# Optimization experiments

Hardware: AMD Instinct MI355X
Metric: run time of the kernel (lower is better)

## Reference

```python
import jax, jax.numpy as jnp
import numpy as np

NUM_HEADS = 16
WINDOW = 64


def setup_inputs() -> dict:
    key = jax.random.key(0)
    ks = jax.random.split(key, 6)
    b, l, d = 2, 2048, 1024
    s = 1.0 / np.sqrt(d)
    return {
        "x": jax.random.normal(ks[0], (b, l, d), dtype=jnp.float32),
        "Wq": jax.random.normal(ks[1], (d, d), dtype=jnp.float32) * s,
        "Wk": jax.random.normal(ks[2], (d, d), dtype=jnp.float32) * s,
        "Wv": jax.random.normal(ks[3], (d, d), dtype=jnp.float32) * s,
        "Wo": jax.random.normal(ks[4], (d, d), dtype=jnp.float32) * s,
        "bo": jax.random.normal(ks[5], (d,), dtype=jnp.float32) * 0.01,
    }


def reference(x, Wq, Wk, Wv, Wo, bo):
    b, l, d = x.shape
    h, w = NUM_HEADS, WINDOW
    dh = d // h
    p = w // 2
    # Projections. Padding is zeros and proj_k/proj_v have no bias, so
    # padding-then-projecting equals projecting-then-zero-padding.
    q = (x @ Wq.T).reshape(b, l, h, dh)                     # (b,l,h,dh)
    xp = jnp.pad(x, ((0, 0), (p, p), (0, 0)))               # (b,l+2p,d)
    k = (xp @ Wk.T).reshape(b, l + 2 * p, h, dh)
    v = (xp @ Wv.T).reshape(b, l + 2 * p, h, dh)
    # Sliding windows: query i attends to padded positions i .. i+w-1
    win_idx = jnp.arange(l)[:, None] + jnp.arange(w)[None, :]  # (l,w)
    kw = k[:, win_idx]                                       # (b,l,w,h,dh)
    vw = v[:, win_idx]                                       # (b,l,w,h,dh)
    scale = 1.0 / np.float32(np.sqrt(dh))
    scores = jnp.einsum('blhd,blwhd->blhw', q, kw) * scale   # (b,l,h,w)
    attn = jax.nn.softmax(scores, axis=-1)
    out = jnp.einsum('blhw,blwhd->blhd', attn, vw).reshape(b, l, d)
    return out @ Wo.T + bo
```

## Files before the change

### kernel.cpp

```cpp
#include <hip/hip_runtime.h>
#include <hip/hip_bf16.h>
#include <cstdint>

typedef __bf16 bf16;
typedef __bf16 bf16x4 __attribute__((ext_vector_type(4)));
typedef __bf16 bf16x8 __attribute__((ext_vector_type(8)));
typedef float floatx4 __attribute__((ext_vector_type(4)));

typedef __attribute__((address_space(1))) void as1_void;
typedef __attribute__((address_space(3))) void as3_void;

__device__ __forceinline__ void gld16(const void* g, void* l) {
#if __has_builtin(__builtin_amdgcn_global_load_lds)
  __builtin_amdgcn_global_load_lds((as1_void*)(uintptr_t)g, (as3_void*)l, 16, 0, 0);
#else
  *(uint4*)l = *(const uint4*)g;
#endif
}

__global__ __launch_bounds__(256) void convert_kernel(
    const float* __restrict__ x, const float* __restrict__ wq,
    const float* __restrict__ wk, const float* __restrict__ wv,
    const float* __restrict__ wo, bf16* __restrict__ xbf,
    bf16* __restrict__ wqkv, bf16* __restrict__ wob) {
  int i = blockIdx.x * 256 + threadIdx.x;
  const float* src;
  bf16* dst;
  int off;
  if (i < 1048576) {
    src = x; dst = xbf; off = i;
  } else if (i < 1310720) {
    src = wq; dst = wqkv; off = i - 1048576;
  } else if (i < 1572864) {
    src = wk; dst = wqkv + 1048576; off = i - 1310720;
  } else if (i < 1835008) {
    src = wv; dst = wqkv + 2097152; off = i - 1572864;
  } else {
    src = wo; dst = wob; off = i - 1835008;
  }
  float4 v = ((const float4*)src)[off];
  bf16x4 o;
  o[0] = (bf16)v.x; o[1] = (bf16)v.y; o[2] = (bf16)v.z; o[3] = (bf16)v.w;
  ((bf16x4*)dst)[off] = o;
}

template <int MODE, int BN>
__global__ __launch_bounds__(256) void gemm_nt(const bf16* __restrict__ A,
                                               const bf16* __restrict__ Bm,
                                               bf16* __restrict__ Cb,
                                               float* __restrict__ Cf,
                                               const float* __restrict__ bias,
                                               int M, int N, int K) {
  constexpr int WN = BN / 2;
  constexpr int NI = WN / 16;
  __shared__ __attribute__((aligned(16))) bf16 As[128 * 32];
  __shared__ __attribute__((aligned(16))) bf16 Bs[BN * 32];
  const int tid = threadIdx.x;
  const int lane = tid & 63;
  const int wave = tid >> 6;
  const int quad = lane >> 4;
  const int n0 = lane & 15;
  const int wm = wave >> 1;
  const int wn = wave & 1;
  const int nwg = gridDim.x * gridDim.y;
  const int nid = blockIdx.y * gridDim.x + blockIdx.x;
  int sid = nid;
  if ((nwg & 7) == 0) sid = (nid & 7) * (nwg >> 3) + (nid >> 3);
  const int bN = sid % gridDim.x, bM = sid / gridDim.x;
  const bf16* Ab = A + (size_t)bM * 128 * K;
  const bf16* Bb = Bm + (size_t)bN * BN * K;
  const int c0 = tid, c1 = tid + 256;
  floatx4 acc[4][NI] = {};
  for (int k0 = 0; k0 < K; k0 += 32) {
    gld16(Ab + (size_t)(c0 >> 2) * K + k0 + (c0 & 3) * 8, &As[c0 * 8]);
    gld16(Ab + (size_t)(c1 >> 2) * K + k0 + (c1 & 3) * 8, &As[c1 * 8]);
#pragma unroll
    for (int cc = 0; cc < BN * 4; cc += 256) {
      const int c = cc + tid;
      gld16(Bb + (size_t)(c >> 2) * K + k0 + (c & 3) * 8, &Bs[c * 8]);
    }
    __syncthreads();
    bf16x8 af[4], bfr[NI];
#pragma unroll
    for (int mi = 0; mi < 4; ++mi)
      af[mi] = *(const bf16x8*)&As[(wm * 64 + mi * 16 + n0) * 32 + quad * 8];
#pragma unroll
    for (int ni = 0; ni < NI; ++ni)
      bfr[ni] = *(const bf16x8*)&Bs[(wn * WN + ni * 16 + n0) * 32 + quad * 8];
#pragma unroll
    for (int mi = 0; mi < 4; ++mi)
#pragma unroll
      for (int ni = 0; ni < NI; ++ni)
        acc[mi][ni] = __builtin_amdgcn_mfma_f32_16x16x32_bf16(
            af[mi], bfr[ni], acc[mi][ni], 0, 0, 0);
    __syncthreads();
  }
  const int rowBase = bM * 128 + wm * 64;
  const int colBase = bN * BN + wn * WN;
#pragma unroll
  for (int ni = 0; ni < NI; ++ni) {
    const int col = colBase + ni * 16 + n0;
    float badd = 0.f;
    if (MODE == 1) badd = bias[col];
#pragma unroll
    for (int mi = 0; mi < 4; ++mi)
#pragma unroll
      for (int r = 0; r < 4; ++r) {
        const int row = rowBase + mi * 16 + quad * 4 + r;
        if (MODE == 0)
          Cb[(size_t)row * N + col] = (bf16)acc[mi][ni][r];
        else
          Cf[(size_t)row * N + col] = acc[mi][ni][r] + badd;
      }
  }
}

#define BAR asm volatile("s_barrier" ::: "memory")
#define LGKM0                                         \
  do {                                                \
    asm volatile("s_waitcnt lgkmcnt(0)" ::: "memory");\
    __builtin_amdgcn_sched_barrier(0);                \
  } while (0)

#define STAGEU(buf, op, u, t)                                                  \
  gld16(((op) ? Bb : Ab) + (size_t)(u) * 64 * Kb + (size_t)(t) * 128 + rowOff, \
        lds + (buf) * 57344 + (op) * 32768 + (u) * 8192 + tid * 16)

#define LDA_(buf, mh)                                                          \
  do {                                                                         \
    _Pragma("unroll") for (int q = 0; q < 4; ++q)                              \
      _Pragma("unroll") for (int ks = 0; ks < 2; ++ks)                         \
        aR[q][ks] = *(const bf16x8*)(lds + (buf) * 57344 +                     \
            (wm * 2 + (mh)) * 8192 + (q * 16 + n0) * 128 +                     \
            ((ks * 64 + quad * 16) ^ swz));                                    \
  } while (0)

#define LDB_(buf, g)                                                           \
  do {                                                                         \
    _Pragma("unroll") for (int j = 0; j < ((g) ? 1 : 2); ++j)                  \
      _Pragma("unroll") for (int ks = 0; ks < 2; ++ks) {                       \
        const int ni_ = (g) ? 2 : j;                                           \
        const int row_ = wn * 48 + ni_ * 16 + n0;                              \
        bR[ni_][ks] = *(const bf16x8*)(lds + (buf) * 57344 + 32768 +           \
            (row_ >> 6) * 8192 + (row_ & 63) * 128 +                           \
            ((ks * 64 + quad * 16) ^ swz));                                    \
      }                                                                        \
  } while (0)

#define MMg0(mh)                                                               \
  do {                                                                         \
    __builtin_amdgcn_s_setprio(1);                                             \
    _Pragma("unroll") for (int q = 0; q < 4; ++q)                              \
      _Pragma("unroll") for (int j = 0; j < 2; ++j)                            \
        _Pragma("unroll") for (int ks = 0; ks < 2; ++ks)                       \
          acc[(mh) * 4 + q][j] = __builtin_amdgcn_mfma_f32_16x16x32_bf16(      \
              aR[q][ks], bR[j][ks], acc[(mh) * 4 + q][j], 0, 0, 0);            \
    __builtin_amdgcn_s_setprio(0);                                             \
  } while (0)

#define MMg1(mh)                                                               \
  do {                                                                         \
    __builtin_amdgcn_s_setprio(1);                                             \
    _Pragma("unroll") for (int q = 0; q < 4; ++q)                              \
      _Pragma("unroll") for (int ks = 0; ks < 2; ++ks)                         \
        acc[(mh) * 4 + q][2] = __builtin_amdgcn_mfma_f32_16x16x32_bf16(        \
            aR[q][ks], bR[2][ks], acc[(mh) * 4 + q][2], 0, 0, 0);              \
    __builtin_amdgcn_s_setprio(0);                                             \
  } while (0)

__global__ __launch_bounds__(512, 2) void gemm192_nt(
    const bf16* __restrict__ A, const bf16* __restrict__ Bm,
    bf16* __restrict__ C, int M, int N, int K) {
  __shared__ __attribute__((aligned(16))) char lds[114688];
  const int tid = threadIdx.x;
  const int lane = tid & 63, wave = tid >> 6;
  const int quad = lane >> 4, n0 = lane & 15;
  const int wm = wave >> 2, wn = wave & 3;
  const int swz = (n0 & 7) << 4;
  const size_t Kb = (size_t)K * 2;
  const char* Ab = (const char*)(A + (size_t)blockIdx.y * 256 * K);
  const char* Bb = (const char*)(Bm + (size_t)blockIdx.x * 192 * K);
  const int srow = tid >> 3;
  const size_t rowOff = (size_t)srow * Kb + (size_t)(16 * ((tid & 7) ^ (srow & 7)));

  floatx4 acc[8][3] = {};
  bf16x8 aR[4][2];
  bf16x8 bR[3][2];

  const int NT = K >> 6;
  const int NI = K >> 7;

  STAGEU(0, 0, 0, 0); STAGEU(0, 0, 1, 0); STAGEU(0, 0, 2, 0); STAGEU(0, 0, 3, 0);
  STAGEU(0, 1, 0, 0); STAGEU(0, 1, 1, 0); STAGEU(0, 1, 2, 0);
  STAGEU(1, 1, 0, 1); STAGEU(1, 1, 1, 1); STAGEU(1, 1, 2, 1);
  STAGEU(1, 0, 0, 1); STAGEU(1, 0, 2, 1);
  asm volatile("s_waitcnt vmcnt(5)" ::: "memory");
  BAR;

  for (int i = 0; i < NI; ++i) {
    const int T = 2 * i;
    const bool s2 = (T + 2 < NT);
    LDB_(0, 0); LDA_(0, 0);
    STAGEU(1, 0, 1, T + 1);
    BAR; LGKM0; MMg0(0); BAR;
    LDB_(0, 1);
    STAGEU(1, 0, 3, T + 1);
    BAR; LGKM0; MMg1(0); BAR;
    LDA_(0, 1);
    if (s2) { STAGEU(0, 1, 0, T + 2); STAGEU(0, 1, 1, T + 2); }
    BAR; LGKM0; MMg0(1); BAR;
    if (s2) STAGEU(0, 1, 2, T + 2);
    BAR; MMg1(1);
    if (i + 1 < NI) { asm volatile("s_waitcnt vmcnt(3)" ::: "memory"); }
    else            { asm volatile("s_waitcnt vmcnt(0)" ::: "memory"); }
    BAR;
    LDB_(1, 0); LDA_(1, 0);
    if (s2) { STAGEU(0, 0, 0, T + 2); STAGEU(0, 0, 2, T + 2); }
    BAR; LGKM0; MMg0(0); BAR;
    LDB_(1, 1);
    if (s2) STAGEU(0, 0, 1, T + 2);
    BAR; LGKM0; MMg1(0); BAR;
    LDA_(1, 1);
    if (s2) { STAGEU(0, 0, 3, T + 2); STAGEU(1, 1, 0, T + 3); }
    BAR; LGKM0; MMg0(1); BAR;
    if (s2) { STAGEU(1, 1, 1, T + 3); STAGEU(1, 1, 2, T + 3);
              STAGEU(1, 0, 0, T + 3); STAGEU(1, 0, 2, T + 3); }
    BAR; MMg1(1);
    asm volatile("s_waitcnt vmcnt(5)" ::: "memory");
    BAR;
  }

  const int rowBase = blockIdx.y * 256 + wm * 128 + quad * 4;
  const int colBase = blockIdx.x * 192 + wn * 48 + n0;
#pragma unroll
  for (int mi = 0; mi < 8; ++mi)
#pragma unroll
    for (int ni = 0; ni < 3; ++ni)
#pragma unroll
      for (int r = 0; r < 4; ++r)
        C[(size_t)(rowBase + mi * 16 + r) * N + colBase + ni * 16] =
            (bf16)acc[mi][ni][r];
}

#undef BAR
#undef LGKM0
#undef STAGEU
#undef LDA_
#undef LDB_
#undef MMg0
#undef MMg1

__global__ __launch_bounds__(256) void attn_kernel(const bf16* __restrict__ qkv,
                                                   bf16* __restrict__ aout) {
  __shared__ __attribute__((aligned(16))) bf16 Ks[128 * 72];
  __shared__ __attribute__((aligned(16))) bf16 VsPs[128 * 72];
  __shared__ __attribute__((aligned(16))) bf16 Vt[64 * 136];
  const int bid = blockIdx.x;
  const int b = bid >> 9;
  const int h = (bid >> 5) & 15;
  const int i0 = (bid & 31) * 64;
  const int tid = threadIdx.x;
  const int wave = tid >> 6, lane = tid & 63;
  const int quad = lane >> 4, n0 = lane & 15;
  bf16* Vs = VsPs;

  bf16x8 aq[2];
#pragma unroll
  for (int ks = 0; ks < 2; ++ks)
    aq[ks] = *(const bf16x8*)(qkv +
        (size_t)(b * 2048 + i0 + wave * 16 + n0) * 3072 + h * 64 + ks * 32 + quad * 8);

#pragma unroll
  for (int it = 0; it < 4; ++it) {
    const int idx = it * 256 + tid;
    const int r = idx >> 3, c = idx & 7;
    const int j = i0 - 32 + r;
    uint4 kv_ = make_uint4(0u, 0u, 0u, 0u);
    uint4 vv = make_uint4(0u, 0u, 0u, 0u);
    if (j >= 0 && j < 2048) {
      const bf16* base = qkv + (size_t)(b * 2048 + j) * 3072 + 1024 + h * 64 + c * 8;
      kv_ = *(const uint4*)base;
      vv = *(const uint4*)(base + 1024);
    }
    *(uint4*)&Ks[r * 72 + c * 8] = kv_;
    *(uint4*)&Vs[r * 72 + c * 8] = vv;
  }
  __syncthreads();

#pragma unroll
  for (int it = 0; it < 4; ++it) {
    const int idx = it * 256 + tid;
    const int t = idx & 127, c = idx >> 7;
    bf16x8 v = *(const bf16x8*)&Vs[t * 72 + c * 8];
#pragma unroll
    for (int jj = 0; jj < 8; ++jj) Vt[(c * 8 + jj) * 136 + t] = v[jj];
  }
  __syncthreads();

  floatx4 accS[8] = {};
#pragma unroll
  for (int nt = 0; nt < 8; ++nt)
#pragma unroll
    for (int ks = 0; ks < 2; ++ks) {
      bf16x8 bk = *(const bf16x8*)&Ks[(nt * 16 + n0) * 72 + ks * 32 + quad * 8];
      accS[nt] = __builtin_amdgcn_mfma_f32_16x16x32_bf16(aq[ks], bk, accS[nt], 0, 0, 0);
    }

  float mrow[4] = {-1e30f, -1e30f, -1e30f, -1e30f};
#pragma unroll
  for (int nt = 0; nt < 8; ++nt)
#pragma unroll
    for (int r = 0; r < 4; ++r) {
      const int q64 = wave * 16 + quad * 4 + r;
      const int t = nt * 16 + n0;
      float s = accS[nt][r] * 0.125f;
      if (t < q64 || t >= q64 + 64) s = -1e30f;
      accS[nt][r] = s;
      mrow[r] = fmaxf(mrow[r], s);
    }
#pragma unroll
  for (int off = 1; off < 16; off <<= 1)
#pragma unroll
    for (int r = 0; r < 4; ++r)
      mrow[r] = fmaxf(mrow[r], __shfl_xor(mrow[r], off));
  float lrow[4] = {0.f, 0.f, 0.f, 0.f};
#pragma unroll
  for (int nt = 0; nt < 8; ++nt)
#pragma unroll
    for (int r = 0; r < 4; ++r) {
      const float e = __expf(accS[nt][r] - mrow[r]);
      accS[nt][r] = e;
      lrow[r] += e;
    }
#pragma unroll
  for (int off = 1; off < 16; off <<= 1)
#pragma unroll
    for (int r = 0; r < 4; ++r) lrow[r] += __shfl_xor(lrow[r], off);

  bf16* Pw = &VsPs[wave * 16 * 136];
#pragma unroll
  for (int r = 0; r < 4; ++r) {
    const float inv = 1.f / lrow[r];
#pragma unroll
    for (int nt = 0; nt < 8; ++nt)
      Pw[(quad * 4 + r) * 136 + nt * 16 + n0] = (bf16)(accS[nt][r] * inv);
  }

  floatx4 accO[4] = {};
#pragma unroll
  for (int kt = 0; kt < 4; ++kt) {
    bf16x8 ap = *(const bf16x8*)&Pw[n0 * 136 + kt * 32 + quad * 8];
#pragma unroll
    for (int dt = 0; dt < 4; ++dt) {
      bf16x8 bv = *(const bf16x8*)&Vt[(dt * 16 + n0) * 136 + kt * 32 + quad * 8];
      accO[dt] = __builtin_amdgcn_mfma_f32_16x16x32_bf16(ap, bv, accO[dt], 0, 0, 0);
    }
  }
#pragma unroll
  for (int dt = 0; dt < 4; ++dt)
#pragma unroll
    for (int r = 0; r < 4; ++r) {
      const int q64 = wave * 16 + quad * 4 + r;
      aout[(size_t)(b * 2048 + i0 + q64) * 1024 + h * 64 + dt * 16 + n0] =
          (bf16)accO[dt][r];
    }
}

extern "C" void kernel_launch(void* const* d_in, const int* in_sizes, int n_in,
                              void* d_out, int out_size, void* d_ws, size_t ws_size,
                              hipStream_t stream) {
  const float* x = (const float*)d_in[0];
  const float* wq = (const float*)d_in[1];
  const float* wk = (const float*)d_in[2];
  const float* wv = (const float*)d_in[3];
  const float* wo = (const float*)d_in[4];
  const float* bo = (const float*)d_in[5];
  char* ws = (char*)d_ws;
  bf16* xbf = (bf16*)(ws);
  bf16* wqkv = (bf16*)(ws + (8u << 20));
  bf16* wob = (bf16*)(ws + (14u << 20));
  bf16* qkv = (bf16*)(ws + (16u << 20));
  bf16* aout = xbf;

  convert_kernel<<<8192, 256, 0, stream>>>(x, wq, wk, wv, wo, xbf, wqkv, wob);
  gemm192_nt<<<dim3(16, 16), 512, 0, stream>>>(xbf, wqkv, qkv, 4096, 3072, 1024);
  attn_kernel<<<1024, 256, 0, stream>>>(qkv, aout);
  gemm_nt<1, 64><<<dim3(16, 32), 256, 0, stream>>>(aout, wob, nullptr,
                                                   (float*)d_out, bo, 4096, 1024,
                                                   1024);
}
```

Measured before the change: 151.3 us.

## Replace output projection GEMM with pipelined swizzled 128x128 tile kernel

Replaces the simple 128x64-tile output projection GEMM, which single-buffers a K=32 slice per step, with a 512-thread 128x128-tile kernel. The new kernel double-buffers K=64 stages in 64 KB of LDS, uses an XOR swizzle against bank conflicts, and interleaves async global-to-LDS loads with MFMA groups at raised wave priority. The goal is to hide memory latency and raise MFMA utilization in the final GEMM. In exchange the grid shrinks to 256 workgroups, and the barrier and vmcnt schedule is intricate and easy to get wrong.

```diff
diff --git a/kernel.cpp b/kernel.cpp
--- a/kernel.cpp
+++ b/kernel.cpp
@@ -42,77 +42,6 @@
   bf16x4 o;
   o[0] = (bf16)v.x; o[1] = (bf16)v.y; o[2] = (bf16)v.z; o[3] = (bf16)v.w;
   ((bf16x4*)dst)[off] = o;
-}
-
-template <int MODE, int BN>
-__global__ __launch_bounds__(256) void gemm_nt(const bf16* __restrict__ A,
-                                               const bf16* __restrict__ Bm,
-                                               bf16* __restrict__ Cb,
-                                               float* __restrict__ Cf,
-                                               const float* __restrict__ bias,
-                                               int M, int N, int K) {
-  constexpr int WN = BN / 2;
-  constexpr int NI = WN / 16;
-  __shared__ __attribute__((aligned(16))) bf16 As[128 * 32];
-  __shared__ __attribute__((aligned(16))) bf16 Bs[BN * 32];
-  const int tid = threadIdx.x;
-  const int lane = tid & 63;
-  const int wave = tid >> 6;
-  const int quad = lane >> 4;
-  const int n0 = lane & 15;
-  const int wm = wave >> 1;
-  const int wn = wave & 1;
-  const int nwg = gridDim.x * gridDim.y;
-  const int nid = blockIdx.y * gridDim.x + blockIdx.x;
-  int sid = nid;
-  if ((nwg & 7) == 0) sid = (nid & 7) * (nwg >> 3) + (nid >> 3);
-  const int bN = sid % gridDim.x, bM = sid / gridDim.x;
-  const bf16* Ab = A + (size_t)bM * 128 * K;
-  const bf16* Bb = Bm + (size_t)bN * BN * K;
-  const int c0 = tid, c1 = tid + 256;
-  floatx4 acc[4][NI] = {};
-  for (int k0 = 0; k0 < K; k0 += 32) {
-    gld16(Ab + (size_t)(c0 >> 2) * K + k0 + (c0 & 3) * 8, &As[c0 * 8]);
-    gld16(Ab + (size_t)(c1 >> 2) * K + k0 + (c1 & 3) * 8, &As[c1 * 8]);
-#pragma unroll
-    for (int cc = 0; cc < BN * 4; cc += 256) {
-      const int c = cc + tid;
-      gld16(Bb + (size_t)(c >> 2) * K + k0 + (c & 3) * 8, &Bs[c * 8]);
-    }
-    __syncthreads();
-    bf16x8 af[4], bfr[NI];
-#pragma unroll
-    for (int mi = 0; mi < 4; ++mi)
-      af[mi] = *(const bf16x8*)&As[(wm * 64 + mi * 16 + n0) * 32 + quad * 8];
-#pragma unroll
-    for (int ni = 0; ni < NI; ++ni)
-      bfr[ni] = *(const bf16x8*)&Bs[(wn * WN + ni * 16 + n0) * 32 + quad * 8];
-#pragma unroll
-    for (int mi = 0; mi < 4; ++mi)
-#pragma unroll
-      for (int ni = 0; ni < NI; ++ni)
-        acc[mi][ni] = __builtin_amdgcn_mfma_f32_16x16x32_bf16(
-            af[mi], bfr[ni], acc[mi][ni], 0, 0, 0);
-    __syncthreads();
-  }
-  const int rowBase = bM * 128 + wm * 64;
-  const int colBase = bN * BN + wn * WN;
-#pragma unroll
-  for (int ni = 0; ni < NI; ++ni) {
-    const int col = colBase + ni * 16 + n0;
-    float badd = 0.f;
-    if (MODE == 1) badd = bias[col];
-#pragma unroll
-    for (int mi = 0; mi < 4; ++mi)
-#pragma unroll
-      for (int r = 0; r < 4; ++r) {
-        const int row = rowBase + mi * 16 + quad * 4 + r;
-        if (MODE == 0)
-          Cb[(size_t)row * N + col] = (bf16)acc[mi][ni][r];
-        else
-          Cf[(size_t)row * N + col] = acc[mi][ni][r] + badd;
-      }
-  }
 }
 
 #define BAR asm volatile("s_barrier" ::: "memory")
@@ -242,13 +171,127 @@
             (bf16)acc[mi][ni][r];
 }
 
-#undef BAR
-#undef LGKM0
 #undef STAGEU
 #undef LDA_
 #undef LDB_
 #undef MMg0
 #undef MMg1
+
+#define STAGE2(buf, op, u, t)                                                  \
+  gld16(((op) ? Bb : Ab) + (size_t)(u) * 64 * Kb + (size_t)(t) * 128 + rowOff, \
+        lds + (buf) * 32768 + (op) * 16384 + (u) * 8192 + tid * 16)
+
+#define LDA2(buf, mh)                                                          \
+  do {                                                                         \
+    _Pragma("unroll") for (int qq = 0; qq < 2; ++qq)                           \
+      _Pragma("unroll") for (int ks = 0; ks < 2; ++ks)                         \
+        aR[qq][ks] = *(const bf16x8*)(lds + (buf) * 32768 + wm * 8192 +        \
+            (((mh) * 2 + qq) * 16 + n0) * 128 + ((ks * 64 + quad * 16) ^ swz));\
+  } while (0)
+
+#define LDB2(buf, j)                                                           \
+  do {                                                                         \
+    _Pragma("unroll") for (int ks = 0; ks < 2; ++ks)                           \
+      bR[j][ks] = *(const bf16x8*)(lds + (buf) * 32768 + 16384 +               \
+          (wn >> 1) * 8192 + ((wn & 1) * 32 + (j) * 16 + n0) * 128 +           \
+          ((ks * 64 + quad * 16) ^ swz));                                      \
+  } while (0)
+
+#define MM2(mh, nh)                                                            \
+  do {                                                                         \
+    __builtin_amdgcn_s_setprio(1);                                             \
+    _Pragma("unroll") for (int qq = 0; qq < 2; ++qq)                           \
+      _Pragma("unroll") for (int ks = 0; ks < 2; ++ks)                         \
+        acc[(mh) * 2 + qq][nh] = __builtin_amdgcn_mfma_f32_16x16x32_bf16(      \
+            aR[qq][ks], bR[nh][ks], acc[(mh) * 2 + qq][nh], 0, 0, 0);          \
+    __builtin_amdgcn_s_setprio(0);                                             \
+  } while (0)
+
+__global__ __launch_bounds__(512, 2) void gemm128_nt(
+    const bf16* __restrict__ A, const bf16* __restrict__ Bm,
+    float* __restrict__ Cf, const float* __restrict__ bias,
+    int M, int N, int K) {
+  __shared__ __attribute__((aligned(16))) char lds[65536];
+  const int tid = threadIdx.x;
+  const int lane = tid & 63, wave = tid >> 6;
+  const int quad = lane >> 4, n0 = lane & 15;
+  const int wm = wave >> 2, wn = wave & 3;
+  const int swz = (n0 & 7) << 4;
+  const size_t Kb = (size_t)K * 2;
+  const int nwg = gridDim.x * gridDim.y;
+  const int nid = blockIdx.y * gridDim.x + blockIdx.x;
+  int sid = nid;
+  if ((nwg & 7) == 0) sid = (nid & 7) * (nwg >> 3) + (nid >> 3);
+  const int bx = sid % gridDim.x, by = sid / gridDim.x;
+  const char* Ab = (const char*)(A + (size_t)by * 128 * K);
+  const char* Bb = (const char*)(Bm + (size_t)bx * 128 * K);
+  const int srow = tid >> 3;
+  const size_t rowOff = (size_t)srow * Kb + (size_t)(16 * ((tid & 7) ^ (srow & 7)));
+
+  floatx4 acc[4][2] = {};
+  bf16x8 aR[2][2];
+  bf16x8 bR[2][2];
+
+  const int NT = K >> 6;
+  const int NI = K >> 7;
+
+  STAGE2(0, 0, 0, 0); STAGE2(0, 0, 1, 0); STAGE2(0, 1, 0, 0); STAGE2(0, 1, 1, 0);
+  STAGE2(1, 1, 0, 1); STAGE2(1, 0, 0, 1);
+  asm volatile("s_waitcnt vmcnt(2)" ::: "memory");
+  BAR;
+
+  for (int i = 0; i < NI; ++i) {
+    const int T = 2 * i;
+    const bool s2 = (T + 2 < NT);
+    LDB2(0, 0); LDA2(0, 0);
+    STAGE2(1, 0, 1, T + 1);
+    BAR; LGKM0; MM2(0, 0); BAR;
+    LDB2(0, 1);
+    STAGE2(1, 1, 1, T + 1);
+    BAR; LGKM0; MM2(0, 1); BAR;
+    LDA2(0, 1);
+    if (s2) STAGE2(0, 1, 0, T + 2);
+    BAR; LGKM0; MM2(1, 0); BAR;
+    if (s2) STAGE2(0, 1, 1, T + 2);
+    BAR; MM2(1, 1);
+    if (i + 1 < NI) { asm volatile("s_waitcnt vmcnt(2)" ::: "memory"); }
+    else            { asm volatile("s_waitcnt vmcnt(0)" ::: "memory"); }
+    BAR;
+    LDB2(1, 0); LDA2(1, 0);
+    if (s2) STAGE2(0, 0, 0, T + 2);
+    BAR; LGKM0; MM2(0, 0); BAR;
+    LDB2(1, 1);
+    if (s2) STAGE2(0, 0, 1, T + 2);
+    BAR; LGKM0; MM2(0, 1); BAR;
+    LDA2(1, 1);
+    if (s2) STAGE2(1, 1, 0, T + 3);
+    BAR; LGKM0; MM2(1, 0); BAR;
+    if (s2) STAGE2(1, 0, 0, T + 3);
+    BAR; MM2(1, 1);
+    asm volatile("s_waitcnt vmcnt(2)" ::: "memory");
+    BAR;
+  }
+
+  const int rowBase = by * 128 + wm * 64 + quad * 4;
+  const int colBase = bx * 128 + wn * 32 + n0;
+#pragma unroll
+  for (int ni = 0; ni < 2; ++ni) {
+    const float badd = bias[colBase + ni * 16];
+#pragma unroll
+    for (int mi = 0; mi < 4; ++mi)
+#pragma unroll
+      for (int r = 0; r < 4; ++r)
+        Cf[(size_t)(rowBase + mi * 16 + r) * N + colBase + ni * 16] =
+            acc[mi][ni][r] + badd;
+  }
+}
+
+#undef BAR
+#undef LGKM0
+#undef STAGE2
+#undef LDA2
+#undef LDB2
+#undef MM2
 
 __global__ __launch_bounds__(256) void attn_kernel(const bf16* __restrict__ qkv,
                                                    bf16* __restrict__ aout) {
@@ -385,7 +428,6 @@
   convert_kernel<<<8192, 256, 0, stream>>>(x, wq, wk, wv, wo, xbf, wqkv, wob);
   gemm192_nt<<<dim3(16, 16), 512, 0, stream>>>(xbf, wqkv, qkv, 4096, 3072, 1024);
   attn_kernel<<<1024, 256, 0, stream>>>(qkv, aout);
-  gemm_nt<1, 64><<<dim3(16, 32), 256, 0, stream>>>(aout, wob, nullptr,
-                                                   (float*)d_out, bo, 4096, 1024,
-                                                   1024);
-}
+  gemm128_nt<<<dim3(8, 32), 512, 0, stream>>>(aout, wob, (float*)d_out, bo,
+                                              4096, 1024, 1024);
+}
```

After: 143.8 us. 1.05x faster.
